# Kernel optimization log

Hardware: AMD Instinct MI355X
Metric: run time of the kernel (lower is better)

## Reference

```python
import jax, jax.numpy as jnp
import numpy as np


def setup_inputs() -> dict:
    key = jax.random.key(0)
    k1, k2 = jax.random.split(key)
    B, T_src, H = 32, 1024, 512
    x = jax.random.normal(k1, (B, T_src, H), dtype=jnp.float32)
    durations = jax.random.randint(k2, (B, T_src), 0, 8, dtype=jnp.int32)
    return {"x": x, "durations": durations}


def reference(x, durations):
    """Length regulator: repeat each source frame x[b, s] durations[b, s] times,
    pad batch to the max expanded length, return (expanded, mel_masks) where
    mel_masks is True at padded positions. Vectorized via cumulative-duration
    searchsorted gather instead of per-batch repeat_interleave.
    x: (B, T_src, H) float, durations: (B, T_src) int.
    """
    B, T_src, H = x.shape
    cum = jnp.cumsum(durations.astype(jnp.int32), axis=1)      # (B, T_src)
    totals = cum[:, -1]                                        # (B,)
    max_len = int(jnp.max(totals))                             # static: concrete inputs
    t = jnp.arange(max_len, dtype=jnp.int32)                   # (T_mel,)
    # src index of output frame t: first s with cum[b, s] > t
    idx = jax.vmap(lambda c: jnp.searchsorted(c, t, side='right'))(cum)  # (B, T_mel)
    idx = jnp.clip(idx, 0, T_src - 1)
    out = jnp.take_along_axis(x, idx[..., None], axis=1)       # (B, T_mel, H)
    mel_masks = t[None, :] >= totals[:, None]                  # (B, T_mel) True = pad
    out = jnp.where(mel_masks[..., None], jnp.zeros((), dtype=x.dtype), out)
    return out, mel_masks
```

## Files before the change

### kernel.cpp

```cpp
#include <hip/hip_runtime.h>


#define B_SZ   32
#define T_SRC  1024
#define H_DIM  512

__global__ void __launch_bounds__(T_SRC) lr_scan_kernel(const int* __restrict__ dur,
                                                        int* __restrict__ cum) {
    __shared__ int s[T_SRC];
    const int b   = blockIdx.x;
    const int tid = threadIdx.x;
    s[tid] = dur[b * T_SRC + tid];
    __syncthreads();
#pragma unroll
    for (int off = 1; off < T_SRC; off <<= 1) {
        int v = (tid >= off) ? s[tid - off] : 0;
        __syncthreads();
        s[tid] += v;
        __syncthreads();
    }
    cum[b * T_SRC + tid] = s[tid];
}

__global__ void __launch_bounds__(128) lr_expand_kernel(const float* __restrict__ x,
                                                        const int* __restrict__ cum,
                                                        float* __restrict__ out,
                                                        float* __restrict__ mask,
                                                        int max_len) {
    const int t   = blockIdx.x;
    const int b   = blockIdx.y;
    const int tid = threadIdx.x;

    const int* c    = cum + b * T_SRC;
    const int total = c[T_SRC - 1];

    float4* out4 = (float4*)(out + ((size_t)b * max_len + t) * H_DIM);

    if (t >= total) {
        if (tid == 0) mask[(size_t)b * max_len + t] = 1.0f;
        out4[tid] = make_float4(0.f, 0.f, 0.f, 0.f);
        return;
    }
    if (tid == 0) mask[(size_t)b * max_len + t] = 0.0f;

    int idx = 0;
#pragma unroll
    for (int sh = 9; sh >= 0; --sh) {
        int probe = idx + (1 << sh);
        if (c[probe - 1] <= t) idx = probe;
    }

    const float4* src4 = (const float4*)(x + ((size_t)b * T_SRC + idx) * H_DIM);
    out4[tid] = src4[tid];
}

extern "C" void kernel_launch(void* const* d_in, const int* in_sizes, int n_in,
                              void* d_out, int out_size, void* d_ws, size_t ws_size,
                              hipStream_t stream) {
    const float* x   = (const float*)d_in[0];
    const int*   dur = (const int*)d_in[1];
    float*       out = (float*)d_out;
    int*         cum = (int*)d_ws;

    const int max_len = out_size / (B_SZ * (H_DIM + 1));
    float* mask = out + (size_t)B_SZ * max_len * H_DIM;

    lr_scan_kernel<<<B_SZ, T_SRC, 0, stream>>>(dur, cum);

    dim3 grid(max_len, B_SZ);
    lr_expand_kernel<<<grid, 128, 0, stream>>>(x, cum, out, mask, max_len);
}
```

Baseline: 324.6 us.

## Replace per-output binary search gather with per-source scatter plus pad kernel

Expansion is now done from the source side: one block per source frame reads its row once and writes it to every output position in its duration range, so the per-output binary search over the cumulative sums goes away. A separate kernel zero-fills the padded frames and sets their mask. This reads x once instead of once per output frame, at the cost of an extra launch, many padded-frame blocks that exit early, and uneven per-block work when durations vary.

```diff
diff --git a/kernel.cpp b/kernel.cpp
--- a/kernel.cpp
+++ b/kernel.cpp
@@ -22,36 +22,41 @@
     cum[b * T_SRC + tid] = s[tid];
 }
 
-__global__ void __launch_bounds__(128) lr_expand_kernel(const float* __restrict__ x,
-                                                        const int* __restrict__ cum,
-                                                        float* __restrict__ out,
-                                                        float* __restrict__ mask,
-                                                        int max_len) {
-    const int t   = blockIdx.x;
+__global__ void __launch_bounds__(128) lr_scatter_kernel(const float* __restrict__ x,
+                                                         const int* __restrict__ cum,
+                                                         float* __restrict__ out,
+                                                         float* __restrict__ mask,
+                                                         int max_len) {
+    const int s   = blockIdx.x;
     const int b   = blockIdx.y;
     const int tid = threadIdx.x;
 
     const int* c    = cum + b * T_SRC;
-    const int total = c[T_SRC - 1];
+    const int end   = c[s];
+    const int start = (s == 0) ? 0 : c[s - 1];
+    if (start == end) return;
 
-    float4* out4 = (float4*)(out + ((size_t)b * max_len + t) * H_DIM);
+    const float4 v = ((const float4*)(x + ((size_t)b * T_SRC + s) * H_DIM))[tid];
+    float* maskb = mask + (size_t)b * max_len;
 
-    if (t >= total) {
-        if (tid == 0) mask[(size_t)b * max_len + t] = 1.0f;
-        out4[tid] = make_float4(0.f, 0.f, 0.f, 0.f);
-        return;
+    for (int t = start; t < end; ++t) {
+        ((float4*)(out + ((size_t)b * max_len + t) * H_DIM))[tid] = v;
+        if (tid == 0) maskb[t] = 0.0f;
     }
-    if (tid == 0) mask[(size_t)b * max_len + t] = 0.0f;
+}
 
-    int idx = 0;
-#pragma unroll
-    for (int sh = 9; sh >= 0; --sh) {
-        int probe = idx + (1 << sh);
-        if (c[probe - 1] <= t) idx = probe;
-    }
+__global__ void __launch_bounds__(128) lr_pad_kernel(const int* __restrict__ cum,
+                                                     float* __restrict__ out,
+                                                     float* __restrict__ mask,
+                                                     int max_len) {
+    const int t     = blockIdx.x;
+    const int b     = blockIdx.y;
+    const int total = cum[b * T_SRC + T_SRC - 1];
+    if (t < total) return;
 
-    const float4* src4 = (const float4*)(x + ((size_t)b * T_SRC + idx) * H_DIM);
-    out4[tid] = src4[tid];
+    ((float4*)(out + ((size_t)b * max_len + t) * H_DIM))[threadIdx.x] =
+        make_float4(0.f, 0.f, 0.f, 0.f);
+    if (threadIdx.x == 0) mask[(size_t)b * max_len + t] = 1.0f;
 }
 
 extern "C" void kernel_launch(void* const* d_in, const int* in_sizes, int n_in,
@@ -67,6 +72,9 @@
 
     lr_scan_kernel<<<B_SZ, T_SRC, 0, stream>>>(dur, cum);
 
-    dim3 grid(max_len, B_SZ);
-    lr_expand_kernel<<<grid, 128, 0, stream>>>(x, cum, out, mask, max_len);
+    dim3 sgrid(T_SRC, B_SZ);
+    lr_scatter_kernel<<<sgrid, 128, 0, stream>>>(x, cum, out, mask, max_len);
+
+    dim3 pgrid(max_len, B_SZ);
+    lr_pad_kernel<<<pgrid, 128, 0, stream>>>(cum, out, mask, max_len);
 }
```

Result: no change. 319.6 us (-1.5%).

## Precompute per-frame source indices in scan kernel; copy rows with persistent waves

Applied to the files above, without the earlier changes.

The scan kernel now scatters each source index over its output frame range into a workspace index buffer and also writes the padding mask. The copy kernel no longer runs a per-frame binary search over the cumulative sums. It uses a fixed grid of 64x32 blocks whose waves each loop over frames, copying a whole 512-float row per wave with two float4 accesses per lane. This removes the per-block search and the tiny 128-thread blocks, at the cost of an extra index-buffer round trip and a serial scatter loop per source frame in the prep kernel.

```diff
diff --git a/kernel.cpp b/kernel.cpp
--- a/kernel.cpp
+++ b/kernel.cpp
@@ -5,8 +5,10 @@
 #define T_SRC  1024
 #define H_DIM  512
 
-__global__ void __launch_bounds__(T_SRC) lr_scan_kernel(const int* __restrict__ dur,
-                                                        int* __restrict__ cum) {
+__global__ void __launch_bounds__(T_SRC) lr_prep(const int* __restrict__ dur,
+                                                 int* __restrict__ idxbuf,
+                                                 float* __restrict__ mask,
+                                                 int max_len) {
     __shared__ int s[T_SRC];
     const int b   = blockIdx.x;
     const int tid = threadIdx.x;
@@ -19,39 +21,41 @@
         s[tid] += v;
         __syncthreads();
     }
-    cum[b * T_SRC + tid] = s[tid];
+    const int end   = s[tid];
+    const int start = tid ? s[tid - 1] : 0;
+    const int total = s[T_SRC - 1];
+
+    int* ib = idxbuf + (size_t)b * max_len;
+    for (int t = start; t < end; ++t) ib[t] = tid;
+    for (int t = total + tid; t < max_len; t += T_SRC) ib[t] = -1;
+    float* mb = mask + (size_t)b * max_len;
+    for (int t = tid; t < max_len; t += T_SRC) mb[t] = (t < total) ? 0.0f : 1.0f;
 }
 
-__global__ void __launch_bounds__(128) lr_expand_kernel(const float* __restrict__ x,
-                                                        const int* __restrict__ cum,
-                                                        float* __restrict__ out,
-                                                        float* __restrict__ mask,
-                                                        int max_len) {
-    const int t   = blockIdx.x;
-    const int b   = blockIdx.y;
-    const int tid = threadIdx.x;
+__global__ void __launch_bounds__(256) lr_copy(const float* __restrict__ x,
+                                               const int* __restrict__ idxbuf,
+                                               float* __restrict__ out,
+                                               int max_len, int nwaves_x) {
+    const int b    = blockIdx.y;
+    const int lane = threadIdx.x & 63;
+    const int wv   = (blockIdx.x << 2) | (threadIdx.x >> 6);
 
-    const int* c    = cum + b * T_SRC;
-    const int total = c[T_SRC - 1];
+    const int*   ib = idxbuf + (size_t)b * max_len;
+    const float* xb = x      + (size_t)b * T_SRC   * H_DIM;
+    float*       ob = out    + (size_t)b * max_len * H_DIM;
 
-    float4* out4 = (float4*)(out + ((size_t)b * max_len + t) * H_DIM);
-
-    if (t >= total) {
-        if (tid == 0) mask[(size_t)b * max_len + t] = 1.0f;
-        out4[tid] = make_float4(0.f, 0.f, 0.f, 0.f);
-        return;
+    for (int t = wv; t < max_len; t += nwaves_x) {
+        const int sidx = ib[t];
+        float4 v0 = make_float4(0.f, 0.f, 0.f, 0.f), v1 = v0;
+        if (sidx >= 0) {
+            const float4* src = (const float4*)(xb + (size_t)sidx * H_DIM);
+            v0 = src[lane];
+            v1 = src[lane + 64];
+        }
+        float4* dst = (float4*)(ob + (size_t)t * H_DIM);
+        dst[lane]      = v0;
+        dst[lane + 64] = v1;
     }
-    if (tid == 0) mask[(size_t)b * max_len + t] = 0.0f;
-
-    int idx = 0;
-#pragma unroll
-    for (int sh = 9; sh >= 0; --sh) {
-        int probe = idx + (1 << sh);
-        if (c[probe - 1] <= t) idx = probe;
-    }
-
-    const float4* src4 = (const float4*)(x + ((size_t)b * T_SRC + idx) * H_DIM);
-    out4[tid] = src4[tid];
 }
 
 extern "C" void kernel_launch(void* const* d_in, const int* in_sizes, int n_in,
@@ -60,13 +64,14 @@
     const float* x   = (const float*)d_in[0];
     const int*   dur = (const int*)d_in[1];
     float*       out = (float*)d_out;
-    int*         cum = (int*)d_ws;
+    int*         idxbuf = (int*)d_ws;
 
     const int max_len = out_size / (B_SZ * (H_DIM + 1));
     float* mask = out + (size_t)B_SZ * max_len * H_DIM;
 
-    lr_scan_kernel<<<B_SZ, T_SRC, 0, stream>>>(dur, cum);
+    lr_prep<<<B_SZ, T_SRC, 0, stream>>>(dur, idxbuf, mask, max_len);
 
-    dim3 grid(max_len, B_SZ);
-    lr_expand_kernel<<<grid, 128, 0, stream>>>(x, cum, out, mask, max_len);
+    const int gx = 64;
+    dim3 grid(gx, B_SZ);
+    lr_copy<<<grid, 256, 0, stream>>>(x, idxbuf, out, max_len, gx * 4);
 }
```

New measurement: 300.5 us. 1.08x faster.
